# Kernel tuning notes

Measured on AMD Instinct MI355X. Metric: run time of the kernel, lower is better.

## Reference

```python
import jax, jax.numpy as jnp
import numpy as np

EPS = 1e-6

def setup_inputs() -> dict:
    key = jax.random.key(0)
    ks = jax.random.split(key, 7)
    T, B, S, A, D = 512, 32, 64, 8, 32
    x = jax.random.normal(ks[0], (T, B, D), dtype=jnp.float32)
    a = jax.random.normal(ks[1], (T, B, A), dtype=jnp.float32)
    mask = jnp.ones((T, B), dtype=jnp.float32)
    mu = jax.random.normal(ks[2], (S, D), dtype=jnp.float32)
    logv = 0.1 * jax.random.normal(ks[3], (S, D), dtype=jnp.float32)
    init_logits = jax.random.normal(ks[4], (S,), dtype=jnp.float32)
    w_base = 0.1 * jax.random.normal(ks[5], (S, S), dtype=jnp.float32)
    w_act = 0.1 * jax.random.normal(ks[6], (A, S, S), dtype=jnp.float32)
    return {"x": x, "a": a, "mask": mask, "mu": mu, "logv": logv,
            "init_logits": init_logits, "w_base": w_base, "w_act": w_act}

def reference(x, a, mask, mu, logv, init_logits, w_base, w_act):
    T, B, D = x.shape
    S = mu.shape[0]
    # Gaussian (diag) emission log-likelihood for every state: [T, B, S]
    var = jnp.exp(logv)
    diff = x[:, :, None, :] - mu  # [T, B, S, D]
    logp_x = -0.5 * jnp.sum(diff * diff / var + logv + jnp.log(2.0 * jnp.pi), axis=-1)
    # Logistic (action-conditioned) transition matrices for t=1..T-1: [T-1, B, S, S]
    trans = jax.nn.softmax(w_base + jnp.einsum('tba,aij->tbij', a[:-1], w_act), axis=-1)
    logp0 = jax.nn.log_softmax(init_logits)
    # alpha_0
    alpha0 = jax.nn.softmax(logp_x[0] + logp0, axis=-1)

    def fwd_step(b, inp):
        tr, lx = inp
        logp_z = jnp.log(jnp.sum(tr * b[:, :, None] + EPS, axis=-2))
        b_new = jax.nn.softmax(lx + logp_z, axis=-1)
        return b_new, b_new

    _, alpha_rest = jax.lax.scan(fwd_step, alpha0, (trans, logp_x[1:]))
    alpha = jnp.concatenate([alpha0[None], alpha_rest], axis=0)  # [T, B, S]

    log_trans = jnp.log(trans + EPS)

    def bwd_step(logb, inp):
        ltr, lx, m = inp
        new = jax.scipy.special.logsumexp(lx[:, None, :] + ltr + logb[:, None, :], axis=-1)
        new = new * (m[:, None] == 1)
        return new, new

    _, lb = jax.lax.scan(bwd_step, jnp.zeros((B, S), x.dtype),
                         (log_trans, logp_x[1:], mask[1:]), reverse=True)
    log_beta = jnp.concatenate([lb, jnp.zeros((1, B, S), x.dtype)], axis=0)  # [T, B, S]

    # Posterior state marginals
    q_z = jax.nn.softmax(jnp.log(alpha + EPS) + log_beta, axis=-1)
    return q_z
```

## Files before the change

kernel.cpp:

```cpp
#include <hip/hip_runtime.h>
#include <math.h>

#define TT 512
#define BB 32
#define SS 64
#define AA 8
#define DD 32
#define EPSF 1e-6f
#define SEPS (64.0f * 1e-6f)
#define TS 68

__device__ __forceinline__ int   f2i(float x){ return __float_as_int(x); }
__device__ __forceinline__ float i2f(int x){ return __int_as_float(x); }
__device__ __forceinline__ float readlane_f(float v, int l){
  return i2f(__builtin_amdgcn_readlane(f2i(v), l));
}
template<int CTRL, int RMASK>
__device__ __forceinline__ float dpp_add(float x){
  return x + i2f(__builtin_amdgcn_update_dpp(0, f2i(x), CTRL, RMASK, 0xf, true));
}
__device__ __forceinline__ float wave_sum_dpp(float x){
  x = dpp_add<0x111, 0xf>(x);
  x = dpp_add<0x112, 0xf>(x);
  x = dpp_add<0x114, 0xf>(x);
  x = dpp_add<0x118, 0xf>(x);
  x = dpp_add<0x142, 0xa>(x);
  x = dpp_add<0x143, 0xc>(x);
  return readlane_f(x, 63);
}
__device__ __forceinline__ float wave_sum(float v){
  #pragma unroll
  for (int m = 1; m < 64; m <<= 1) v += __shfl_xor(v, m, 64);
  return v;
}
__device__ __forceinline__ float wave_max(float v){
  #pragma unroll
  for (int m = 1; m < 64; m <<= 1) v = fmaxf(v, __shfl_xor(v, m, 64));
  return v;
}
#define BARRIER() asm volatile("s_waitcnt lgkmcnt(0)\n\ts_barrier" ::: "memory")

__global__ void prep_kernel(const float* __restrict__ logv,
                            float* __restrict__ iv, float* __restrict__ cs){
  int gid = blockIdx.x * blockDim.x + threadIdx.x;
  if (gid < SS * DD) iv[gid] = __expf(-logv[gid]);
  if (gid < SS){
    float s = 0.f;
    #pragma unroll
    for (int d = 0; d < DD; ++d) s += logv[gid * DD + d];
    cs[gid] = s + (float)DD * 1.8378770664093453f;
  }
}

__global__ __launch_bounds__(256) void logpx_kernel(
    const float* __restrict__ x, const float* __restrict__ mu,
    const float* __restrict__ iv, const float* __restrict__ cs,
    float* __restrict__ slx_out){
  const int lane = threadIdx.x & 63;
  const int w = threadIdx.x >> 6;
  const int row = blockIdx.x * 4 + w;
  const float* __restrict__ xp  = x  + row * DD;
  const float* __restrict__ mup = mu + lane * DD;
  const float* __restrict__ ivp = iv + lane * DD;
  float acc = 0.f;
  #pragma unroll
  for (int d = 0; d < DD; ++d){
    float diff = xp[d] - mup[d];
    acc = fmaf(diff * diff, ivp[d], acc);
  }
  float lx = -0.5f * (acc + cs[lane]);
  float mx = wave_max(lx);
  slx_out[row * SS + lane] = lx - mx;
}

__global__ __launch_bounds__(512) void trans_kernel(
    const float* __restrict__ a, const float* __restrict__ w_base,
    const float* __restrict__ w_act, float* __restrict__ trans){
  const int b  = blockIdx.x >> 4;
  const int tc = blockIdx.x & 15;
  const int t0 = tc * 32;
  const int tid = threadIdx.x;
  const int i  = tid >> 3;
  const int j0 = (tid & 7) * 8;
  __shared__ float aS[32 * 8];
  if (tid < 256)
    aS[tid] = a[(((t0 + (tid >> 3)) * BB) + b) * AA + (tid & 7)];
  float wb[8], wa[8][8];
  #pragma unroll
  for (int jj = 0; jj < 8; ++jj){
    wb[jj] = w_base[i * SS + j0 + jj];
    #pragma unroll
    for (int k = 0; k < 8; ++k)
      wa[k][jj] = w_act[(k * SS + i) * SS + j0 + jj];
  }
  __syncthreads();
  const int nt = ((TT - 1) - t0 < 32) ? ((TT - 1) - t0) : 32;
  for (int tt = 0; tt < nt; ++tt){
    float aa[8];
    #pragma unroll
    for (int k = 0; k < 8; ++k) aa[k] = aS[tt * 8 + k];
    float ev[8]; float rs = 0.f;
    #pragma unroll
    for (int jj = 0; jj < 8; ++jj){
      float u = wb[jj];
      #pragma unroll
      for (int k = 0; k < 8; ++k) u = fmaf(aa[k], wa[k][jj], u);
      ev[jj] = __expf(u); rs += ev[jj];
    }
    rs += __shfl_xor(rs, 1, 64);
    rs += __shfl_xor(rs, 2, 64);
    rs += __shfl_xor(rs, 4, 64);
    float rinv = __builtin_amdgcn_rcpf(rs);
    float* __restrict__ op = trans + ((size_t)(t0 + tt) * BB + b) * (SS * SS)
                           + i * SS + j0;
    *(float4*)op       = make_float4(ev[0]*rinv, ev[1]*rinv, ev[2]*rinv, ev[3]*rinv);
    *(float4*)(op + 4) = make_float4(ev[4]*rinv, ev[5]*rinv, ev[6]*rinv, ev[7]*rinv);
  }
}

__global__ __launch_bounds__(512) void scan_pre_kernel(
    const float* __restrict__ slx, const float* __restrict__ mask,
    const float* __restrict__ il, const float* __restrict__ trans,
    float* __restrict__ alpha, float* __restrict__ log_beta){
  const int lane = threadIdx.x & 63;
  const int w    = threadIdx.x >> 6;
  const bool is_fwd = (blockIdx.x < BB);
  const int b = is_fwd ? blockIdx.x : (blockIdx.x - BB);

  __shared__ __align__(16) float tile[3][SS * TS];
  __shared__ float fpart[2][4][SS];
  __shared__ float mLDS[TT];

  for (int idx = threadIdx.x; idx < TT; idx += 512)
    mLDS[idx] = mask[idx * BB + b];

  if (w >= 4){
    const int pw = w - 4;
    const size_t thofs  = (size_t)pw * 1024 + (size_t)lane * 16;
    const int    ldsoff = (pw * 16 + (lane >> 2)) * TS + (lane & 3) * 16;
    const size_t tstride = (size_t)BB * SS * SS;
    const float* gb = trans + (size_t)b * (SS * SS) + thofs;
    const long gstep = is_fwd ? (long)tstride : -(long)tstride;
    const float* g0 = is_fwd ? gb : (gb + (size_t)(TT - 2) * tstride);
    float4 A0,A1,A2,A3, B0,B1,B2,B3;
    {
      const float4* gp = (const float4*)g0;
      float4 c0 = gp[0], c1 = gp[1], c2 = gp[2], c3 = gp[3];
      const float4* ga = (const float4*)(g0 + gstep);
      A0 = ga[0]; A1 = ga[1]; A2 = ga[2]; A3 = ga[3];
      const float4* gbp = (const float4*)(g0 + 2 * gstep);
      B0 = gbp[0]; B1 = gbp[1]; B2 = gbp[2]; B3 = gbp[3];
      float* tp = &tile[0][ldsoff];
      *(float4*)tp = c0; *(float4*)(tp+4) = c1;
      *(float4*)(tp+8) = c2; *(float4*)(tp+12) = c3;
    }
    const float* gcur = g0 + 3 * gstep;
    BARRIER();
    int tw = 1;
    for (int s = 0; s < TT - 1; ++s){
      if (s <= TT - 3){
        float* tp = &tile[tw][ldsoff];
        if ((s & 1) == 0){
          *(float4*)tp = A0; *(float4*)(tp+4) = A1;
          *(float4*)(tp+8) = A2; *(float4*)(tp+12) = A3;
          if (s <= TT - 5){
            const float4* gp = (const float4*)gcur;
            A0 = gp[0]; A1 = gp[1]; A2 = gp[2]; A3 = gp[3];
            gcur += gstep;
          }
        } else {
          *(float4*)tp = B0; *(float4*)(tp+4) = B1;
          *(float4*)(tp+8) = B2; *(float4*)(tp+12) = B3;
          if (s <= TT - 5){
            const float4* gp = (const float4*)gcur;
            B0 = gp[0]; B1 = gp[1]; B2 = gp[2]; B3 = gp[3];
            gcur += gstep;
          }
        }
        tw = (tw == 2) ? 0 : tw + 1;
      }
      BARRIER();
    }
  } else if (is_fwd){
    const int wb16 = __builtin_amdgcn_readfirstlane(w * 16);
    float u = __expf(slx[b * SS + lane] + il[lane]);
    float c = __builtin_amdgcn_rcpf(wave_sum_dpp(u));
    if (w == 0) alpha[b * SS + lane] = u * c;
    float slxn = slx[(BB + b) * SS + lane];
    float elxc = 0.f;
    BARRIER();
    int ts = 0;
    for (int s = 0; s < TT - 1; ++s){
      if (s > 0){
        const int fs = (s - 1) & 1;
        float S = (fpart[fs][0][lane] + fpart[fs][1][lane])
                + (fpart[fs][2][lane] + fpart[fs][3][lane]);
        u = elxc * fmaf(c, S, SEPS);
        c = __builtin_amdgcn_rcpf(wave_sum_dpp(u));
        if (w == 0) alpha[(s * BB + b) * SS + lane] = u * c;
      }
      float va = u;
      const float* __restrict__ tp = &tile[ts][0];
      float a0 = 0.f, a1 = 0.f, a2 = 0.f, a3 = 0.f;
      #pragma unroll
      for (int r = 0; r < 16; r += 4){
        a0 = fmaf(readlane_f(va, wb16 + r    ), tp[(wb16 + r    ) * TS + lane], a0);
        a1 = fmaf(readlane_f(va, wb16 + r + 1), tp[(wb16 + r + 1) * TS + lane], a1);
        a2 = fmaf(readlane_f(va, wb16 + r + 2), tp[(wb16 + r + 2) * TS + lane], a2);
        a3 = fmaf(readlane_f(va, wb16 + r + 3), tp[(wb16 + r + 3) * TS + lane], a3);
      }
      fpart[s & 1][w][lane] = (a0 + a1) + (a2 + a3);
      elxc = __expf(slxn);
      if (s + 2 <= TT - 1) slxn = slx[((s + 2) * BB + b) * SS + lane];
      ts = (ts == 2) ? 0 : ts + 1;
      BARRIER();
    }
    {
      const int fs = (TT - 2) & 1;
      float S = (fpart[fs][0][lane] + fpart[fs][1][lane])
              + (fpart[fs][2][lane] + fpart[fs][3][lane]);
      u = elxc * fmaf(c, S, SEPS);
      c = __builtin_amdgcn_rcpf(wave_sum_dpp(u));
      if (w == 0) alpha[((TT - 1) * BB + b) * SS + lane] = u * c;
    }
  } else {
    const int wb16 = __builtin_amdgcn_readfirstlane(w * 16);
    float breg = 0.f, rWc = 1.f;
    if (w == 0) log_beta[((TT - 1) * BB + b) * SS + lane] = 0.f;
    float slxc = slx[((TT - 1) * BB + b) * SS + lane];
    float mprev = 1.f;
    BARRIER();
    int ts = 0;
    for (int s = 0; s < TT - 1; ++s){
      if (s > 0){
        const int fs = (s - 1) & 1;
        float eh = (fpart[fs][0][lane] + fpart[fs][1][lane])
                 + (fpart[fs][2][lane] + fpart[fs][3][lane]);
        float v = __logf(fmaf(eh, rWc, EPSF));
        breg = (mprev == 1.0f) ? v : 0.0f;
        if (w == 0) log_beta[((TT - 1 - s) * BB + b) * SS + lane] = breg;
      }
      float wgt = __expf(slxc + breg);
      float W = wave_sum_dpp(wgt);
      rWc = __builtin_amdgcn_rcpf(W);
      const float* __restrict__ tp = &tile[ts][lane * TS + wb16];
      float4 e0 = *(const float4*)(tp);
      float4 e1 = *(const float4*)(tp + 4);
      float4 e2 = *(const float4*)(tp + 8);
      float4 e3 = *(const float4*)(tp + 12);
      float a0 = 0.f, a1 = 0.f, a2 = 0.f, a3 = 0.f;
      a0 = fmaf(readlane_f(wgt, wb16 + 0),  e0.x, a0);
      a1 = fmaf(readlane_f(wgt, wb16 + 1),  e0.y, a1);
      a2 = fmaf(readlane_f(wgt, wb16 + 2),  e0.z, a2);
      a3 = fmaf(readlane_f(wgt, wb16 + 3),  e0.w, a3);
      a0 = fmaf(readlane_f(wgt, wb16 + 4),  e1.x, a0);
      a1 = fmaf(readlane_f(wgt, wb16 + 5),  e1.y, a1);
      a2 = fmaf(readlane_f(wgt, wb16 + 6),  e1.z, a2);
      a3 = fmaf(readlane_f(wgt, wb16 + 7),  e1.w, a3);
      a0 = fmaf(readlane_f(wgt, wb16 + 8),  e2.x, a0);
      a1 = fmaf(readlane_f(wgt, wb16 + 9),  e2.y, a1);
      a2 = fmaf(readlane_f(wgt, wb16 + 10), e2.z, a2);
      a3 = fmaf(readlane_f(wgt, wb16 + 11), e2.w, a3);
      a0 = fmaf(readlane_f(wgt, wb16 + 12), e3.x, a0);
      a1 = fmaf(readlane_f(wgt, wb16 + 13), e3.y, a1);
      a2 = fmaf(readlane_f(wgt, wb16 + 14), e3.z, a2);
      a3 = fmaf(readlane_f(wgt, wb16 + 15), e3.w, a3);
      fpart[s & 1][w][lane] = (a0 + a1) + (a2 + a3);
      mprev = mLDS[TT - 1 - s];
      if (s <= TT - 3) slxc = slx[((TT - 2 - s) * BB + b) * SS + lane];
      ts = (ts == 2) ? 0 : ts + 1;
      BARRIER();
    }
    {
      const int fs = (TT - 2) & 1;
      float eh = (fpart[fs][0][lane] + fpart[fs][1][lane])
               + (fpart[fs][2][lane] + fpart[fs][3][lane]);
      float v = __logf(fmaf(eh, rWc, EPSF));
      breg = (mprev == 1.0f) ? v : 0.0f;
      if (w == 0) log_beta[b * SS + lane] = breg;
    }
  }
}

__global__ __launch_bounds__(768) void scan_kernel(
    const float* __restrict__ slx, const float* __restrict__ mask,
    const float* __restrict__ il, const float* __restrict__ a,
    const float* __restrict__ w_base, const float* __restrict__ w_act,
    float* __restrict__ alpha, float* __restrict__ log_beta){
  const int lane = threadIdx.x & 63;
  const int w    = threadIdx.x >> 6;
  const bool is_fwd = (blockIdx.x < BB);
  const int b = is_fwd ? blockIdx.x : (blockIdx.x - BB);

  __shared__ __align__(16) float tile[3][SS * TS];
  __shared__ float rsp[3][8][SS];
  __shared__ float fpart[2][4][SS];
  __shared__ __align__(16) float aLDS[TT * AA];
  __shared__ float mLDS[TT];

  for (int idx = threadIdx.x; idx < TT * AA; idx += 768){
    int t = idx >> 3, k = idx & 7;
    aLDS[idx] = a[(t * BB + b) * AA + k];
  }
  for (int idx = threadIdx.x; idx < TT; idx += 768)
    mLDS[idx] = mask[idx * BB + b];

  if (w >= 4){
    const int pw = w - 4;
    const int jb = pw * 8;
    float wb[8], wa[8][8];
    #pragma unroll
    for (int jj = 0; jj < 8; ++jj){
      wb[jj] = w_base[lane * SS + jb + jj];
      #pragma unroll
      for (int k = 0; k < 8; ++k)
        wa[k][jj] = w_act[(k * SS + lane) * SS + jb + jj];
    }
    float aa[8], aan[8];
    {
      const int t0 = is_fwd ? 0 : (TT - 2);
      const float* __restrict__ ap = a + (t0 * BB + b) * AA;
      #pragma unroll
      for (int k = 0; k < 8; ++k) aa[k] = ap[k];
      const int t1 = is_fwd ? 1 : (TT - 3);
      const float* __restrict__ ap1 = a + (t1 * BB + b) * AA;
      #pragma unroll
      for (int k = 0; k < 8; ++k) aan[k] = ap1[k];
    }
    {
      float ev[8]; float racc = 0.f;
      #pragma unroll
      for (int jj = 0; jj < 8; ++jj){
        float u = wb[jj];
        #pragma unroll
        for (int k = 0; k < 8; ++k) u = fmaf(aa[k], wa[k][jj], u);
        ev[jj] = __expf(u); racc += ev[jj];
      }
      *(float4*)&tile[0][lane * TS + jb]     = make_float4(ev[0],ev[1],ev[2],ev[3]);
      *(float4*)&tile[0][lane * TS + jb + 4] = make_float4(ev[4],ev[5],ev[6],ev[7]);
      rsp[0][pw][lane] = racc;
    }
    BARRIER();
    int tw = 1;
    for (int s = 0; s < TT - 1; ++s){
      if (s <= TT - 3){
        #pragma unroll
        for (int k = 0; k < 8; ++k) aa[k] = aan[k];
        if (s + 1 <= TT - 3){
          const int tn = is_fwd ? (s + 2) : (TT - 4 - s);
          #pragma unroll
          for (int k = 0; k < 8; ++k) aan[k] = aLDS[tn * AA + k];
        }
        float ev[8]; float racc = 0.f;
        #pragma unroll
        for (int jj = 0; jj < 8; ++jj){
          float u = wb[jj];
          #pragma unroll
          for (int k = 0; k < 8; ++k) u = fmaf(aa[k], wa[k][jj], u);
          ev[jj] = __expf(u); racc += ev[jj];
        }
        *(float4*)&tile[tw][lane * TS + jb]     = make_float4(ev[0],ev[1],ev[2],ev[3]);
        *(float4*)&tile[tw][lane * TS + jb + 4] = make_float4(ev[4],ev[5],ev[6],ev[7]);
        rsp[tw][pw][lane] = racc;
        tw = (tw == 2) ? 0 : tw + 1;
      }
      BARRIER();
    }
  } else if (is_fwd){
    const int wb16 = __builtin_amdgcn_readfirstlane(w * 16);
    float u = __expf(slx[b * SS + lane] + il[lane]);
    float c = __builtin_amdgcn_rcpf(wave_sum_dpp(u));
    if (w == 0) alpha[b * SS + lane] = u * c;
    float slxn = slx[(BB + b) * SS + lane];
    float elxc = 0.f;
    BARRIER();
    int ts = 0;
    for (int s = 0; s < TT - 1; ++s){
      if (s > 0){
        const int fs = (s - 1) & 1;
        float S = (fpart[fs][0][lane] + fpart[fs][1][lane])
                + (fpart[fs][2][lane] + fpart[fs][3][lane]);
        u = elxc * fmaf(c, S, SEPS);
        c = __builtin_amdgcn_rcpf(wave_sum_dpp(u));
        if (w == 0) alpha[(s * BB + b) * SS + lane] = u * c;
      }
      float rs = ((rsp[ts][0][lane] + rsp[ts][1][lane]) + (rsp[ts][2][lane] + rsp[ts][3][lane]))
               + ((rsp[ts][4][lane] + rsp[ts][5][lane]) + (rsp[ts][6][lane] + rsp[ts][7][lane]));
      float va = u * __builtin_amdgcn_rcpf(rs);
      const float* __restrict__ tp = &tile[ts][0];
      float a0 = 0.f, a1 = 0.f, a2 = 0.f, a3 = 0.f;
      #pragma unroll
      for (int r = 0; r < 16; r += 4){
        a0 = fmaf(readlane_f(va, wb16 + r    ), tp[(wb16 + r    ) * TS + lane], a0);
        a1 = fmaf(readlane_f(va, wb16 + r + 1), tp[(wb16 + r + 1) * TS + lane], a1);
        a2 = fmaf(readlane_f(va, wb16 + r + 2), tp[(wb16 + r + 2) * TS + lane], a2);
        a3 = fmaf(readlane_f(va, wb16 + r + 3), tp[(wb16 + r + 3) * TS + lane], a3);
      }
      fpart[s & 1][w][lane] = (a0 + a1) + (a2 + a3);
      elxc = __expf(slxn);
      if (s + 2 <= TT - 1) slxn = slx[((s + 2) * BB + b) * SS + lane];
      ts = (ts == 2) ? 0 : ts + 1;
      BARRIER();
    }
    {
      const int fs = (TT - 2) & 1;
      float S = (fpart[fs][0][lane] + fpart[fs][1][lane])
              + (fpart[fs][2][lane] + fpart[fs][3][lane]);
      u = elxc * fmaf(c, S, SEPS);
      c = __builtin_amdgcn_rcpf(wave_sum_dpp(u));
      if (w == 0) alpha[((TT - 1) * BB + b) * SS + lane] = u * c;
    }
  } else {
    const int wb16 = __builtin_amdgcn_readfirstlane(w * 16);
    float breg = 0.f, rWc = 1.f;
    if (w == 0) log_beta[((TT - 1) * BB + b) * SS + lane] = 0.f;
    float slxc = slx[((TT - 1) * BB + b) * SS + lane];
    float mprev = 1.f;
    BARRIER();
    int ts = 0, pts = 2;
    for (int s = 0; s < TT - 1; ++s){
      if (s > 0){
        const int fs = (s - 1) & 1;
        float eh = (fpart[fs][0][lane] + fpart[fs][1][lane])
                 + (fpart[fs][2][lane] + fpart[fs][3][lane]);
        float rsv = ((rsp[pts][0][lane] + rsp[pts][1][lane]) + (rsp[pts][2][lane] + rsp[pts][3][lane]))
                  + ((rsp[pts][4][lane] + rsp[pts][5][lane]) + (rsp[pts][6][lane] + rsp[pts][7][lane]));
        float v = __logf(fmaf(eh * __builtin_amdgcn_rcpf(rsv), rWc, EPSF));
        breg = (mprev == 1.0f) ? v : 0.0f;
        if (w == 0) log_beta[((TT - 1 - s) * BB + b) * SS + lane] = breg;
      }
      float wgt = __expf(slxc + breg);
      float W = wave_sum_dpp(wgt);
      rWc = __builtin_amdgcn_rcpf(W);
      const float* __restrict__ tp = &tile[ts][lane * TS + wb16];
      float4 e0 = *(const float4*)(tp);
      float4 e1 = *(const float4*)(tp + 4);
      float4 e2 = *(const float4*)(tp + 8);
      float4 e3 = *(const float4*)(tp + 12);
      float a0 = 0.f, a1 = 0.f, a2 = 0.f, a3 = 0.f;
      a0 = fmaf(readlane_f(wgt, wb16 + 0),  e0.x, a0);
      a1 = fmaf(readlane_f(wgt, wb16 + 1),  e0.y, a1);
      a2 = fmaf(readlane_f(wgt, wb16 + 2),  e0.z, a2);
      a3 = fmaf(readlane_f(wgt, wb16 + 3),  e0.w, a3);
      a0 = fmaf(readlane_f(wgt, wb16 + 4),  e1.x, a0);
      a1 = fmaf(readlane_f(wgt, wb16 + 5),  e1.y, a1);
      a2 = fmaf(readlane_f(wgt, wb16 + 6),  e1.z, a2);
      a3 = fmaf(readlane_f(wgt, wb16 + 7),  e1.w, a3);
      a0 = fmaf(readlane_f(wgt, wb16 + 8),  e2.x, a0);
      a1 = fmaf(readlane_f(wgt, wb16 + 9),  e2.y, a1);
      a2 = fmaf(readlane_f(wgt, wb16 + 10), e2.z, a2);
      a3 = fmaf(readlane_f(wgt, wb16 + 11), e2.w, a3);
      a0 = fmaf(readlane_f(wgt, wb16 + 12), e3.x, a0);
      a1 = fmaf(readlane_f(wgt, wb16 + 13), e3.y, a1);
      a2 = fmaf(readlane_f(wgt, wb16 + 14), e3.z, a2);
      a3 = fmaf(readlane_f(wgt, wb16 + 15), e3.w, a3);
      fpart[s & 1][w][lane] = (a0 + a1) + (a2 + a3);
      mprev = mLDS[TT - 1 - s];
      if (s <= TT - 3) slxc = slx[((TT - 2 - s) * BB + b) * SS + lane];
      pts = ts; ts = (ts == 2) ? 0 : ts + 1;
      BARRIER();
    }
    {
      const int fs = (TT - 2) & 1;
      float eh = (fpart[fs][0][lane] + fpart[fs][1][lane])
               + (fpart[fs][2][lane] + fpart[fs][3][lane]);
      float rsv = ((rsp[pts][0][lane] + rsp[pts][1][lane]) + (rsp[pts][2][lane] + rsp[pts][3][lane]))
                + ((rsp[pts][4][lane] + rsp[pts][5][lane]) + (rsp[pts][6][lane] + rsp[pts][7][lane]));
      float v = __logf(fmaf(eh * __builtin_amdgcn_rcpf(rsv), rWc, EPSF));
      breg = (mprev == 1.0f) ? v : 0.0f;
      if (w == 0) log_beta[b * SS + lane] = breg;
    }
  }
}

__global__ __launch_bounds__(256) void qz_kernel(
    const float* __restrict__ alpha, const float* __restrict__ log_beta,
    float* __restrict__ out){
  const int lane = threadIdx.x & 63;
  const int w = threadIdx.x >> 6;
  const int row = blockIdx.x * 4 + w;
  float v = __logf(alpha[row * SS + lane] + EPSF) + log_beta[row * SS + lane];
  float mx = wave_max(v);
  float e = __expf(v - mx);
  float sm = wave_sum(e);
  out[row * SS + lane] = e * __builtin_amdgcn_rcpf(sm);
}

extern "C" void kernel_launch(void* const* d_in, const int* in_sizes, int n_in,
                              void* d_out, int out_size, void* d_ws, size_t ws_size,
                              hipStream_t stream){
  const float* x      = (const float*)d_in[0];
  const float* a      = (const float*)d_in[1];
  const float* mask   = (const float*)d_in[2];
  const float* mu     = (const float*)d_in[3];
  const float* logv   = (const float*)d_in[4];
  const float* il     = (const float*)d_in[5];
  const float* w_base = (const float*)d_in[6];
  const float* w_act  = (const float*)d_in[7];
  float* out = (float*)d_out;

  float* ws = (float*)d_ws;
  const size_t TBS = (size_t)TT * BB * SS;
  float* iv       = ws;
  float* cs       = ws + 2048;
  float* slx      = ws + 4096;
  float* alpha    = slx + TBS;
  float* log_beta = alpha + TBS;
  float* trans    = log_beta + TBS;

  const size_t TRANS_FLOATS = (size_t)(TT - 1) * BB * SS * SS;
  const size_t need_bytes = ((size_t)4096 + 3 * TBS + TRANS_FLOATS) * sizeof(float);

  prep_kernel<<<8, 256, 0, stream>>>(logv, iv, cs);
  logpx_kernel<<<TT * BB / 4, 256, 0, stream>>>(x, mu, iv, cs, slx);
  if (ws_size >= need_bytes){
    trans_kernel<<<512, 512, 0, stream>>>(a, w_base, w_act, trans);
    scan_pre_kernel<<<2 * BB, 512, 0, stream>>>(slx, mask, il, trans,
                                                alpha, log_beta);
  } else {
    scan_kernel<<<2 * BB, 768, 0, stream>>>(slx, mask, il, a, w_base, w_act,
                                            alpha, log_beta);
  }
  qz_kernel<<<TT * BB / 4, 256, 0, stream>>>(alpha, log_beta, out);
}
```

Measured before the change: 403.2 us.

## Store precomputed transition matrices in fp16 and merge producer into compute waves

The transition softmax output is now written as packed fp16 in a swizzled layout, which halves the global traffic the scan kernels stream. The scan kernel drops its four dedicated loader waves: each of the four compute waves loads its own 16-row slice, converts it to fp32 into the LDS ring, and prefetches three steps ahead. The block shrinks from 512 to 256 threads. Storing probabilities in fp16 costs accuracy, and the loads and conversions now sit on the serial critical path of each step.

Measured after the change: 587.9 us. 1.46x slower.

```diff
diff --git a/kernel.cpp b/kernel.cpp
--- a/kernel.cpp
+++ b/kernel.cpp
@@ -1,4 +1,5 @@
 #include <hip/hip_runtime.h>
+#include <hip/hip_fp16.h>
 #include <math.h>
 
 #define TT 512
@@ -39,6 +40,17 @@
   return v;
 }
 #define BARRIER() asm volatile("s_waitcnt lgkmcnt(0)\n\ts_barrier" ::: "memory")
+
+__device__ __forceinline__ unsigned pk2(float a, float b){
+  return (unsigned)__half_as_ushort(__float2half_rn(a))
+       | ((unsigned)__half_as_ushort(__float2half_rn(b)) << 16);
+}
+__device__ __forceinline__ float uplo(unsigned u){
+  return __half2float(__ushort_as_half((unsigned short)(u & 0xffffu)));
+}
+__device__ __forceinline__ float uphi(unsigned u){
+  return __half2float(__ushort_as_half((unsigned short)(u >> 16)));
+}
 
 __global__ void prep_kernel(const float* __restrict__ logv,
                             float* __restrict__ iv, float* __restrict__ cs){
@@ -75,7 +87,7 @@
 
 __global__ __launch_bounds__(512) void trans_kernel(
     const float* __restrict__ a, const float* __restrict__ w_base,
-    const float* __restrict__ w_act, float* __restrict__ trans){
+    const float* __restrict__ w_act, unsigned short* __restrict__ trans, int F){
   const int b  = blockIdx.x >> 4;
   const int tc = blockIdx.x & 15;
   const int t0 = tc * 32;
@@ -94,7 +106,9 @@
       wa[k][jj] = w_act[(k * SS + i) * SS + j0 + jj];
   }
   __syncthreads();
-  const int nt = ((TT - 1) - t0 < 32) ? ((TT - 1) - t0) : 32;
+  const int swofs = (j0 >> 4) * 1024 + i * 16 + (j0 & 15);
+  int rem = F - t0;
+  const int nt = (rem < 0) ? 0 : (rem < 32 ? rem : 32);
   for (int tt = 0; tt < nt; ++tt){
     float aa[8];
     #pragma unroll
@@ -111,19 +125,32 @@
     rs += __shfl_xor(rs, 2, 64);
     rs += __shfl_xor(rs, 4, 64);
     float rinv = __builtin_amdgcn_rcpf(rs);
-    float* __restrict__ op = trans + ((size_t)(t0 + tt) * BB + b) * (SS * SS)
-                           + i * SS + j0;
-    *(float4*)op       = make_float4(ev[0]*rinv, ev[1]*rinv, ev[2]*rinv, ev[3]*rinv);
-    *(float4*)(op + 4) = make_float4(ev[4]*rinv, ev[5]*rinv, ev[6]*rinv, ev[7]*rinv);
-  }
-}
-
-__global__ __launch_bounds__(512) void scan_pre_kernel(
+    unsigned short* __restrict__ op = trans
+        + ((size_t)(t0 + tt) * BB + b) * (SS * SS) + swofs;
+    uint4 o;
+    o.x = pk2(ev[0]*rinv, ev[1]*rinv);
+    o.y = pk2(ev[2]*rinv, ev[3]*rinv);
+    o.z = pk2(ev[4]*rinv, ev[5]*rinv);
+    o.w = pk2(ev[6]*rinv, ev[7]*rinv);
+    *(uint4*)op = o;
+  }
+}
+
+#define STORE16(SLOT, PA, PB) do{ \
+  float* tp_ = &tile[SLOT][lane * TS + wb16]; \
+  *(float4*)(tp_)      = make_float4(uplo(PA.x), uphi(PA.x), uplo(PA.y), uphi(PA.y)); \
+  *(float4*)(tp_ + 4)  = make_float4(uplo(PA.z), uphi(PA.z), uplo(PA.w), uphi(PA.w)); \
+  *(float4*)(tp_ + 8)  = make_float4(uplo(PB.x), uphi(PB.x), uplo(PB.y), uphi(PB.y)); \
+  *(float4*)(tp_ + 12) = make_float4(uplo(PB.z), uphi(PB.z), uplo(PB.w), uphi(PB.w)); \
+}while(0)
+
+__global__ __launch_bounds__(256) void scan_stream_kernel(
     const float* __restrict__ slx, const float* __restrict__ mask,
-    const float* __restrict__ il, const float* __restrict__ trans,
+    const float* __restrict__ il, const unsigned short* __restrict__ trans,
     float* __restrict__ alpha, float* __restrict__ log_beta){
   const int lane = threadIdx.x & 63;
   const int w    = threadIdx.x >> 6;
+  const int wb16 = __builtin_amdgcn_readfirstlane(w * 16);
   const bool is_fwd = (blockIdx.x < BB);
   const int b = is_fwd ? blockIdx.x : (blockIdx.x - BB);
 
@@ -131,66 +158,60 @@
   __shared__ float fpart[2][4][SS];
   __shared__ float mLDS[TT];
 
-  for (int idx = threadIdx.x; idx < TT; idx += 512)
-    mLDS[idx] = mask[idx * BB + b];
-
-  if (w >= 4){
-    const int pw = w - 4;
-    const size_t thofs  = (size_t)pw * 1024 + (size_t)lane * 16;
-    const int    ldsoff = (pw * 16 + (lane >> 2)) * TS + (lane & 3) * 16;
-    const size_t tstride = (size_t)BB * SS * SS;
-    const float* gb = trans + (size_t)b * (SS * SS) + thofs;
-    const long gstep = is_fwd ? (long)tstride : -(long)tstride;
-    const float* g0 = is_fwd ? gb : (gb + (size_t)(TT - 2) * tstride);
-    float4 A0,A1,A2,A3, B0,B1,B2,B3;
-    {
-      const float4* gp = (const float4*)g0;
-      float4 c0 = gp[0], c1 = gp[1], c2 = gp[2], c3 = gp[3];
-      const float4* ga = (const float4*)(g0 + gstep);
-      A0 = ga[0]; A1 = ga[1]; A2 = ga[2]; A3 = ga[3];
-      const float4* gbp = (const float4*)(g0 + 2 * gstep);
-      B0 = gbp[0]; B1 = gbp[1]; B2 = gbp[2]; B3 = gbp[3];
-      float* tp = &tile[0][ldsoff];
-      *(float4*)tp = c0; *(float4*)(tp+4) = c1;
-      *(float4*)(tp+8) = c2; *(float4*)(tp+12) = c3;
-    }
-    const float* gcur = g0 + 3 * gstep;
-    BARRIER();
-    int tw = 1;
-    for (int s = 0; s < TT - 1; ++s){
-      if (s <= TT - 3){
-        float* tp = &tile[tw][ldsoff];
-        if ((s & 1) == 0){
-          *(float4*)tp = A0; *(float4*)(tp+4) = A1;
-          *(float4*)(tp+8) = A2; *(float4*)(tp+12) = A3;
-          if (s <= TT - 5){
-            const float4* gp = (const float4*)gcur;
-            A0 = gp[0]; A1 = gp[1]; A2 = gp[2]; A3 = gp[3];
-            gcur += gstep;
-          }
-        } else {
-          *(float4*)tp = B0; *(float4*)(tp+4) = B1;
-          *(float4*)(tp+8) = B2; *(float4*)(tp+12) = B3;
-          if (s <= TT - 5){
-            const float4* gp = (const float4*)gcur;
-            B0 = gp[0]; B1 = gp[1]; B2 = gp[2]; B3 = gp[3];
-            gcur += gstep;
-          }
-        }
-        tw = (tw == 2) ? 0 : tw + 1;
-      }
-      BARRIER();
-    }
-  } else if (is_fwd){
-    const int wb16 = __builtin_amdgcn_readfirstlane(w * 16);
-    float u = __expf(slx[b * SS + lane] + il[lane]);
-    float c = __builtin_amdgcn_rcpf(wave_sum_dpp(u));
+  if (!is_fwd)
+    for (int idx = threadIdx.x; idx < TT; idx += 256)
+      mLDS[idx] = mask[idx * BB + b];
+
+  const long BBSSh = (long)BB * SS * SS;
+  const long d = is_fwd ? 1 : -1;
+  const int t0 = is_fwd ? 0 : (TT - 2);
+  const unsigned short* __restrict__ gbh =
+      trans + (size_t)b * (SS * SS) + w * 1024 + lane * 16;
+  {
+    const unsigned short* p = gbh + (long)t0 * BBSSh;
+    uint4 Pa = *(const uint4*)p; uint4 Pb = *(const uint4*)(p + 8);
+    STORE16(0, Pa, Pb);
+  }
+  uint4 Aa, Ab, Ba, Bb, Ca, Cb;
+  { const unsigned short* p = gbh + (long)(t0 +     d) * BBSSh; Aa = *(const uint4*)p; Ab = *(const uint4*)(p + 8); }
+  { const unsigned short* p = gbh + (long)(t0 + 2 * d) * BBSSh; Ba = *(const uint4*)p; Bb = *(const uint4*)(p + 8); }
+  { const unsigned short* p = gbh + (long)(t0 + 3 * d) * BBSSh; Ca = *(const uint4*)p; Cb = *(const uint4*)(p + 8); }
+  const unsigned short* pc = gbh + (long)(t0 + 4 * d) * BBSSh;
+  const long pstep = d * BBSSh;
+
+  float u = 0.f, c = 0.f, elxc = 0.f, slxn = 0.f;
+  float breg = 0.f, rWc = 1.f, slxc = 0.f, mprev = 1.f;
+  if (is_fwd){
+    u = __expf(slx[b * SS + lane] + il[lane]);
+    c = __builtin_amdgcn_rcpf(wave_sum_dpp(u));
     if (w == 0) alpha[b * SS + lane] = u * c;
-    float slxn = slx[(BB + b) * SS + lane];
-    float elxc = 0.f;
-    BARRIER();
-    int ts = 0;
-    for (int s = 0; s < TT - 1; ++s){
+    slxn = slx[(BB + b) * SS + lane];
+  } else {
+    if (w == 0) log_beta[((TT - 1) * BB + b) * SS + lane] = 0.f;
+    slxc = slx[((TT - 1) * BB + b) * SS + lane];
+  }
+  int ts = 0, tw = 1, par = 0;
+  BARRIER();
+
+  for (int s = 0; s < TT - 1; ++s){
+    if (s <= TT - 3){
+      if (par == 0){
+        STORE16(tw, Aa, Ab);
+        if (s <= TT - 6){ Aa = *(const uint4*)pc; Ab = *(const uint4*)(pc + 8); pc += pstep; }
+      } else if (par == 1){
+        STORE16(tw, Ba, Bb);
+        if (s <= TT - 6){ Ba = *(const uint4*)pc; Bb = *(const uint4*)(pc + 8); pc += pstep; }
+      } else {
+        STORE16(tw, Ca, Cb);
+        if (s <= TT - 6){ Ca = *(const uint4*)pc; Cb = *(const uint4*)(pc + 8); pc += pstep; }
+      }
+      par = (par == 2) ? 0 : par + 1;
+    }
+    if (is_fwd){
+      const float* __restrict__ tp = &tile[ts][0];
+      float tv[16];
+      #pragma unroll
+      for (int r = 0; r < 16; ++r) tv[r] = tp[(wb16 + r) * TS + lane];
       if (s > 0){
         const int fs = (s - 1) & 1;
         float S = (fpart[fs][0][lane] + fpart[fs][1][lane])
@@ -199,39 +220,23 @@
         c = __builtin_amdgcn_rcpf(wave_sum_dpp(u));
         if (w == 0) alpha[(s * BB + b) * SS + lane] = u * c;
       }
-      float va = u;
-      const float* __restrict__ tp = &tile[ts][0];
       float a0 = 0.f, a1 = 0.f, a2 = 0.f, a3 = 0.f;
       #pragma unroll
       for (int r = 0; r < 16; r += 4){
-        a0 = fmaf(readlane_f(va, wb16 + r    ), tp[(wb16 + r    ) * TS + lane], a0);
-        a1 = fmaf(readlane_f(va, wb16 + r + 1), tp[(wb16 + r + 1) * TS + lane], a1);
-        a2 = fmaf(readlane_f(va, wb16 + r + 2), tp[(wb16 + r + 2) * TS + lane], a2);
-        a3 = fmaf(readlane_f(va, wb16 + r + 3), tp[(wb16 + r + 3) * TS + lane], a3);
+        a0 = fmaf(readlane_f(u, wb16 + r    ), tv[r    ], a0);
+        a1 = fmaf(readlane_f(u, wb16 + r + 1), tv[r + 1], a1);
+        a2 = fmaf(readlane_f(u, wb16 + r + 2), tv[r + 2], a2);
+        a3 = fmaf(readlane_f(u, wb16 + r + 3), tv[r + 3], a3);
       }
       fpart[s & 1][w][lane] = (a0 + a1) + (a2 + a3);
       elxc = __expf(slxn);
       if (s + 2 <= TT - 1) slxn = slx[((s + 2) * BB + b) * SS + lane];
-      ts = (ts == 2) ? 0 : ts + 1;
-      BARRIER();
-    }
-    {
-      const int fs = (TT - 2) & 1;
-      float S = (fpart[fs][0][lane] + fpart[fs][1][lane])
-              + (fpart[fs][2][lane] + fpart[fs][3][lane]);
-      u = elxc * fmaf(c, S, SEPS);
-      c = __builtin_amdgcn_rcpf(wave_sum_dpp(u));
-      if (w == 0) alpha[((TT - 1) * BB + b) * SS + lane] = u * c;
-    }
-  } else {
-    const int wb16 = __builtin_amdgcn_readfirstlane(w * 16);
-    float breg = 0.f, rWc = 1.f;
-    if (w == 0) log_beta[((TT - 1) * BB + b) * SS + lane] = 0.f;
-    float slxc = slx[((TT - 1) * BB + b) * SS + lane];
-    float mprev = 1.f;
-    BARRIER();
-    int ts = 0;
-    for (int s = 0; s < TT - 1; ++s){
+    } else {
+      const float* __restrict__ tp = &tile[ts][lane * TS + wb16];
+      float4 e0 = *(const float4*)(tp);
+      float4 e1 = *(const float4*)(tp + 4);
+      float4 e2 = *(const float4*)(tp + 8);
+      float4 e3 = *(const float4*)(tp + 12);
       if (s > 0){
         const int fs = (s - 1) & 1;
         float eh = (fpart[fs][0][lane] + fpart[fs][1][lane])
@@ -243,11 +248,6 @@
       float wgt = __expf(slxc + breg);
       float W = wave_sum_dpp(wgt);
       rWc = __builtin_amdgcn_rcpf(W);
-      const float* __restrict__ tp = &tile[ts][lane * TS + wb16];
-      float4 e0 = *(const float4*)(tp);
-      float4 e1 = *(const float4*)(tp + 4);
-      float4 e2 = *(const float4*)(tp + 8);
-      float4 e3 = *(const float4*)(tp + 12);
       float a0 = 0.f, a1 = 0.f, a2 = 0.f, a3 = 0.f;
       a0 = fmaf(readlane_f(wgt, wb16 + 0),  e0.x, a0);
       a1 = fmaf(readlane_f(wgt, wb16 + 1),  e0.y, a1);
@@ -268,17 +268,24 @@
       fpart[s & 1][w][lane] = (a0 + a1) + (a2 + a3);
       mprev = mLDS[TT - 1 - s];
       if (s <= TT - 3) slxc = slx[((TT - 2 - s) * BB + b) * SS + lane];
-      ts = (ts == 2) ? 0 : ts + 1;
-      BARRIER();
-    }
-    {
-      const int fs = (TT - 2) & 1;
-      float eh = (fpart[fs][0][lane] + fpart[fs][1][lane])
-               + (fpart[fs][2][lane] + fpart[fs][3][lane]);
-      float v = __logf(fmaf(eh, rWc, EPSF));
-      breg = (mprev == 1.0f) ? v : 0.0f;
-      if (w == 0) log_beta[b * SS + lane] = breg;
-    }
+    }
+    tw = (tw == 2) ? 0 : tw + 1; ts = (ts == 2) ? 0 : ts + 1;
+    BARRIER();
+  }
+  if (is_fwd){
+    const int fs = (TT - 2) & 1;
+    float S = (fpart[fs][0][lane] + fpart[fs][1][lane])
+            + (fpart[fs][2][lane] + fpart[fs][3][lane]);
+    u = elxc * fmaf(c, S, SEPS);
+    c = __builtin_amdgcn_rcpf(wave_sum_dpp(u));
+    if (w == 0) alpha[((TT - 1) * BB + b) * SS + lane] = u * c;
+  } else {
+    const int fs = (TT - 2) & 1;
+    float eh = (fpart[fs][0][lane] + fpart[fs][1][lane])
+             + (fpart[fs][2][lane] + fpart[fs][3][lane]);
+    float v = __logf(fmaf(eh, rWc, EPSF));
+    breg = (mprev == 1.0f) ? v : 0.0f;
+    if (w == 0) log_beta[b * SS + lane] = breg;
   }
 }
 
@@ -506,17 +513,17 @@
   float* slx      = ws + 4096;
   float* alpha    = slx + TBS;
   float* log_beta = alpha + TBS;
-  float* trans    = log_beta + TBS;
-
-  const size_t TRANS_FLOATS = (size_t)(TT - 1) * BB * SS * SS;
-  const size_t need_bytes = ((size_t)4096 + 3 * TBS + TRANS_FLOATS) * sizeof(float);
+  unsigned short* trans = (unsigned short*)(log_beta + TBS);
+
+  const size_t base_bytes = ((size_t)4096 + 3 * TBS) * 4;
+  const size_t full_bytes = base_bytes + (size_t)(TT - 1) * BB * SS * SS * 2;
 
   prep_kernel<<<8, 256, 0, stream>>>(logv, iv, cs);
   logpx_kernel<<<TT * BB / 4, 256, 0, stream>>>(x, mu, iv, cs, slx);
-  if (ws_size >= need_bytes){
-    trans_kernel<<<512, 512, 0, stream>>>(a, w_base, w_act, trans);
-    scan_pre_kernel<<<2 * BB, 512, 0, stream>>>(slx, mask, il, trans,
-                                                alpha, log_beta);
+  if (ws_size >= full_bytes){
+    trans_kernel<<<512, 512, 0, stream>>>(a, w_base, w_act, trans, TT - 1);
+    scan_stream_kernel<<<2 * BB, 256, 0, stream>>>(slx, mask, il, trans,
+                                                   alpha, log_beta);
   } else {
     scan_kernel<<<2 * BB, 768, 0, stream>>>(slx, mask, il, a, w_base, w_act,
                                             alpha, log_beta);
```
